# Performance work log

Measured on AMD Instinct MI355X. Metric: run time of the kernel, lower is better.

Reference implementation:

```python
import jax, jax.numpy as jnp
import numpy as np
from jax import lax

N, D, H, C = 4096, 1024, 512, 21  # rois, head feat dim, gcn hidden, n_classes


def setup_inputs() -> dict:
    key = jax.random.key(0)
    ks = jax.random.split(key, 9)
    x1 = jax.random.uniform(ks[0], (N,), minval=0.0, maxval=800.0)
    y1 = jax.random.uniform(ks[1], (N,), minval=0.0, maxval=800.0)
    w = jax.random.uniform(ks[2], (N,), minval=16.0, maxval=256.0)
    h = jax.random.uniform(ks[3], (N,), minval=16.0, maxval=256.0)
    rois = jnp.stack([x1, y1, x1 + w, y1 + h], axis=1)  # [N,4] x1,y1,x2,y2
    pooled_feat = jax.random.normal(ks[4], (N, D))
    Wg1 = jax.random.normal(ks[5], (D, H)) * 0.02
    bg1 = jnp.zeros((H,), jnp.float32)
    Wg2 = jax.random.normal(ks[6], (H, H)) * 0.02
    bg2 = jnp.zeros((H,), jnp.float32)
    W_bbox = jax.random.normal(ks[7], (H, 4 * C)) * 0.001
    b_bbox = jnp.zeros((4 * C,), jnp.float32)
    W_cls = jax.random.normal(ks[8], (H, C)) * 0.01
    b_cls = jnp.zeros((C,), jnp.float32)
    return dict(rois=rois, pooled_feat=pooled_feat, Wg1=Wg1, bg1=bg1, Wg2=Wg2,
                bg2=bg2, W_bbox=W_bbox, b_bbox=b_bbox, W_cls=W_cls, b_cls=b_cls)


def _iou_binary_adj(boxes):
    # bbox_overlaps_batch IoU (Pascal +1 convention), then binarize and zero diag
    x1, y1, x2, y2 = boxes[:, 0], boxes[:, 1], boxes[:, 2], boxes[:, 3]
    area = (x2 - x1 + 1.0) * (y2 - y1 + 1.0)
    iw = jnp.maximum(jnp.minimum(x2[:, None], x2[None, :]) - jnp.maximum(x1[:, None], x1[None, :]) + 1.0, 0.0)
    ih = jnp.maximum(jnp.minimum(y2[:, None], y2[None, :]) - jnp.maximum(y1[:, None], y1[None, :]) + 1.0, 0.0)
    inter = iw * ih
    iou = inter / (area[:, None] + area[None, :] - inter)
    adj = (iou > 0.0).astype(boxes.dtype)
    return adj * (1.0 - jnp.eye(boxes.shape[0], dtype=boxes.dtype))


def _connected_components(adj):
    # jit-friendly replacement for DFS subgraph_split: min-label propagation
    # with pointer jumping (converges in O(log diameter) iterations).
    n = adj.shape[0]
    labels0 = jnp.arange(n, dtype=jnp.int32)
    big = jnp.int32(n)

    def step(labels, _):
        nb = jnp.min(jnp.where(adj > 0.0, labels[None, :], big), axis=1)
        labels = jnp.minimum(labels, nb)
        labels = labels[labels]  # pointer jump
        return labels, None

    labels, _ = lax.scan(step, labels0, None, length=32)
    return labels  # component id per roi (min vertex index in component)


def _cosine_adj(x):
    # pairwise cosine similarity, diag zeroed (matches s != t loop)
    xn = x / jnp.maximum(jnp.linalg.norm(x, axis=1, keepdims=True), 1e-6)
    a = xn @ xn.T
    return a * (1.0 - jnp.eye(x.shape[0], dtype=x.dtype))


def reference(rois, pooled_feat, Wg1, bg1, Wg2, bg2, W_bbox, b_bbox, W_cls, b_cls):
    adj_bin = _iou_binary_adj(rois)          # [N,N] 0/1
    labels = _connected_components(adj_bin)  # [N] int32 subgraph ids
    A = _cosine_adj(pooled_feat)             # [N,N]
    h1 = jax.nn.relu(A @ (pooled_feat @ Wg1) + bg1)  # GCN layer 1
    h2 = jax.nn.relu(A @ (h1 @ Wg2) + bg2)           # GCN layer 2
    bbox_pred = h2 @ W_bbox + b_bbox          # [N, 4*C]
    cls_prob = jax.nn.softmax(h2 @ W_cls + b_cls, axis=1)  # [N, C]
    return labels, cls_prob, bbox_pred
```

## Files before the change

kernel.cpp:

```cpp
#include <hip/hip_runtime.h>
#include <hip/hip_bf16.h>
#include <stdint.h>


typedef __attribute__((ext_vector_type(8))) short short8;
typedef __attribute__((ext_vector_type(4))) float floatx4;

#define BK 64
#define LSTR 72

__device__ __forceinline__ unsigned short bfbits(float f) {
  union { float f; unsigned int i; } u; u.f = f;
  unsigned int r = u.i + 0x7fffu + ((u.i >> 16) & 1);
  return (unsigned short)(r >> 16);
}

template <int MODE>
__global__ __launch_bounds__(256) void gemm64(
    const __hip_bfloat16* __restrict__ P, const __hip_bfloat16* __restrict__ Q,
    int KC, int ld, int N, float* __restrict__ part,
    const float* __restrict__ rinorm, const __hip_bfloat16* __restrict__ ST,
    const float* __restrict__ bias, __hip_bfloat16* __restrict__ outb,
    float* __restrict__ outf, float* __restrict__ cls, const float* __restrict__ bias2) {
  __shared__ short As[2][64 * LSTR];
  __shared__ short Bs[2][64 * LSTR];
  const int tid = threadIdx.x;
  const int w = tid >> 6, lane = tid & 63;
  const size_t m0 = (size_t)blockIdx.y * 64, n0 = (size_t)blockIdx.x * 64;
  const int z = blockIdx.z;

  const int srow = tid >> 2, skoff = (tid & 3) * 16;
  const short* gA = (const short*)P + (m0 + srow) * (size_t)ld + (size_t)z * KC + skoff;
  const short* gB = (const short*)Q + (n0 + srow) * (size_t)ld + (size_t)z * KC + skoff;
  const int soff = srow * LSTR + skoff;

  const int wm = (w >> 1) * 32, wn = (w & 1) * 32;
  const int lr = lane & 15, ko = (lane >> 4) * 8;

  floatx4 acc[2][2];
#pragma unroll
  for (int i = 0; i < 2; ++i)
#pragma unroll
    for (int j = 0; j < 2; ++j) acc[i][j] = (floatx4){0.f, 0.f, 0.f, 0.f};

  const int nIter = KC / BK;
  short8 ra0 = *(const short8*)gA;
  short8 ra1 = *(const short8*)(gA + 8);
  short8 rb0 = *(const short8*)gB;
  short8 rb1 = *(const short8*)(gB + 8);
  *(short8*)&As[0][soff] = ra0;
  *(short8*)&As[0][soff + 8] = ra1;
  *(short8*)&Bs[0][soff] = rb0;
  *(short8*)&Bs[0][soff + 8] = rb1;
  if (nIter > 1) {
    ra0 = *(const short8*)(gA + BK);
    ra1 = *(const short8*)(gA + BK + 8);
    rb0 = *(const short8*)(gB + BK);
    rb1 = *(const short8*)(gB + BK + 8);
  }
  __syncthreads();

  for (int it = 0; it < nIter; ++it) {
    const int cur = it & 1;
    short8 av[2][2], bv[2][2];
#pragma unroll
    for (int ks = 0; ks < 2; ++ks)
#pragma unroll
      for (int t = 0; t < 2; ++t) {
        av[ks][t] = *(const short8*)&As[cur][(wm + t * 16 + lr) * LSTR + ks * 32 + ko];
        bv[ks][t] = *(const short8*)&Bs[cur][(wn + t * 16 + lr) * LSTR + ks * 32 + ko];
      }
    if (it + 1 < nIter) {
      *(short8*)&As[cur ^ 1][soff] = ra0;
      *(short8*)&As[cur ^ 1][soff + 8] = ra1;
      *(short8*)&Bs[cur ^ 1][soff] = rb0;
      *(short8*)&Bs[cur ^ 1][soff + 8] = rb1;
      if (it + 2 < nIter) {
        const int off = (it + 2) * BK;
        ra0 = *(const short8*)(gA + off);
        ra1 = *(const short8*)(gA + off + 8);
        rb0 = *(const short8*)(gB + off);
        rb1 = *(const short8*)(gB + off + 8);
      }
    }
#pragma unroll
    for (int ks = 0; ks < 2; ++ks)
#pragma unroll
      for (int i = 0; i < 2; ++i)
#pragma unroll
        for (int j = 0; j < 2; ++j)
          acc[i][j] = __builtin_amdgcn_mfma_f32_16x16x32_bf16(av[ks][i], bv[ks][j], acc[i][j], 0, 0, 0);
    __syncthreads();
  }

  const size_t MN = (size_t)(gridDim.y * 64) * (size_t)N;
  float* cp = part + (size_t)z * MN;
  float* lg = (float*)&As[0][0];
  const int rb4 = (lane >> 4) * 4;
#pragma unroll
  for (int i = 0; i < 2; ++i)
#pragma unroll
    for (int j = 0; j < 2; ++j)
#pragma unroll
      for (int r = 0; r < 4; ++r) {
        int row = (int)m0 + wm + i * 16 + rb4 + r;
        int col = (int)n0 + wn + j * 16 + lr;
        float v = acc[i][j][r];
        if (MODE == 0) {
          cp[(size_t)row * N + col] = v;
        } else if (MODE == 1) {
          outb[(size_t)row * 4096 + col] = __float2bfloat16(v);
        } else if (MODE == 2) {
          v = rinorm[row] * v - __bfloat162float(ST[(size_t)col * 4096 + row]) + bias[col];
          outb[(size_t)row * 512 + col] = __float2bfloat16(fmaxf(v, 0.f));
        } else {
          if (blockIdx.x == 0) {
            outf[(size_t)row * 84 + col] = v + bias[col];
          } else {
            int lrow = wm + i * 16 + rb4 + r;
            if (col < 84) outf[(size_t)row * 84 + col] = v + bias[col];
            else if (col < 105) lg[lrow * 22 + (col - 84)] = v + bias2[col - 84];
          }
        }
      }
  if (MODE == 3) {
    __syncthreads();
    if (blockIdx.x == 1 && tid < 64) {
      const float* Lr = &lg[tid * 22];
      float m = Lr[0];
#pragma unroll
      for (int k = 1; k < 21; ++k) m = fmaxf(m, Lr[k]);
      float s = 0.f;
      float e[21];
#pragma unroll
      for (int k = 0; k < 21; ++k) { e[k] = expf(Lr[k] - m); s += e[k]; }
      float inv = 1.f / s;
      float* dst = &cls[(m0 + tid) * 21];
#pragma unroll
      for (int k = 0; k < 21; ++k) dst[k] = e[k] * inv;
    }
  }
}

__global__ void k_red0(const float* __restrict__ part, __hip_bfloat16* __restrict__ out,
                       int n, int ns) {
  int i = (blockIdx.x * 256 + threadIdx.x) * 4;
  if (i >= n) return;
  float4 v = *(const float4*)(part + i);
  for (int s = 1; s < ns; ++s) {
    float4 q = *(const float4*)(part + (size_t)s * n + i);
    v.x += q.x; v.y += q.y; v.z += q.z; v.w += q.w;
  }
  out[i] = __float2bfloat16(v.x);
  out[i + 1] = __float2bfloat16(v.y);
  out[i + 2] = __float2bfloat16(v.z);
  out[i + 3] = __float2bfloat16(v.w);
}

__global__ void k_nf_adj(const float* __restrict__ X, __hip_bfloat16* __restrict__ Xb,
                         float* __restrict__ rinorm, const float4* __restrict__ rois,
                         unsigned long long* __restrict__ adj, int* __restrict__ labels) {
  int blk = blockIdx.x, tid = threadIdx.x;
  int lane = tid & 63;
  if (blk < 1024) {
    int wave = (blk * 256 + tid) >> 6;
    const float4* row = (const float4*)(X + (size_t)wave * 1024);
    uint2* orow = (uint2*)((short*)Xb + (size_t)wave * 1024);
    float s = 0.f;
#pragma unroll
    for (int it = 0; it < 4; ++it) {
      float4 p = row[lane + it * 64];
      s += p.x * p.x + p.y * p.y + p.z * p.z + p.w * p.w;
      uint2 q;
      q.x = (unsigned int)bfbits(p.x) | ((unsigned int)bfbits(p.y) << 16);
      q.y = (unsigned int)bfbits(p.z) | ((unsigned int)bfbits(p.w) << 16);
      orow[lane + it * 64] = q;
    }
    for (int o = 32; o; o >>= 1) s += __shfl_down(s, o);
    if (lane == 0) rinorm[wave] = 1.f / fmaxf(sqrtf(s), 1e-6f);
  } else {
    int node = ((blk - 1024) * 256 + tid) >> 6;
    float4 bi = rois[node];
    unsigned long long myword = 0;
    int mn = node;
    for (int w = 0; w < 64; ++w) {
      int j = w * 64 + lane;
      float4 bj = rois[j];
      float iw = fminf(bi.z, bj.z) - fmaxf(bi.x, bj.x) + 1.0f;
      float ih = fminf(bi.w, bj.w) - fmaxf(bi.y, bj.y) + 1.0f;
      bool ov = (iw > 0.f) && (ih > 0.f) && (j != node);
      unsigned long long msk = __ballot(ov);
      if (lane == w) myword = msk;
      if (msk) mn = min(mn, w * 64 + (int)__builtin_ctzll(msk));
    }
    adj[(size_t)node * 64 + lane] = myword;
    if (lane == 0) labels[node] = mn;
  }
}

__global__ void k_prep(const __hip_bfloat16* __restrict__ Xb, const float* __restrict__ rinorm,
                       const float* __restrict__ Wg1, const float* __restrict__ Wg2,
                       const float* __restrict__ Wb, const float* __restrict__ Wc,
                       __hip_bfloat16* __restrict__ XRT, __hip_bfloat16* __restrict__ Wg1T,
                       __hip_bfloat16* __restrict__ Wg2T, __hip_bfloat16* __restrict__ WcatT) {
  __shared__ float s[32][33];
  const int tid = threadIdx.x;
  const int tx = tid & 31, ty = tid >> 5;
  int blk = blockIdx.x;
  if (blk < 4096) {
    int c0 = (blk & 31) * 32, r0 = (blk >> 5) * 32;
#pragma unroll
    for (int k = 0; k < 4; ++k) {
      int r = r0 + ty + k * 8;
      s[ty + k * 8][tx] = __bfloat162float(Xb[(size_t)r * 1024 + c0 + tx]) * rinorm[r];
    }
    __syncthreads();
#pragma unroll
    for (int k = 0; k < 4; ++k)
      XRT[(size_t)(c0 + ty + k * 8) * 4096 + r0 + tx] = __float2bfloat16(s[tx][ty + k * 8]);
  } else if (blk < 4608) {
    int l = blk - 4096;
    int c0 = (l & 15) * 32, r0 = (l >> 4) * 32;
#pragma unroll
    for (int k = 0; k < 4; ++k)
      s[ty + k * 8][tx] = Wg1[(size_t)(r0 + ty + k * 8) * 512 + c0 + tx];
    __syncthreads();
#pragma unroll
    for (int k = 0; k < 4; ++k)
      Wg1T[(size_t)(c0 + ty + k * 8) * 1024 + r0 + tx] = __float2bfloat16(s[tx][ty + k * 8]);
  } else if (blk < 4864) {
    int l = blk - 4608;
    int c0 = (l & 15) * 32, r0 = (l >> 4) * 32;
#pragma unroll
    for (int k = 0; k < 4; ++k)
      s[ty + k * 8][tx] = Wg2[(size_t)(r0 + ty + k * 8) * 512 + c0 + tx];
    __syncthreads();
#pragma unroll
    for (int k = 0; k < 4; ++k)
      Wg2T[(size_t)(c0 + ty + k * 8) * 512 + r0 + tx] = __float2bfloat16(s[tx][ty + k * 8]);
  } else {
    int idx = (blk - 4864) * 256 + tid;
    int r = idx >> 9, k = idx & 511;
    float v = 0.f;
    if (r < 84) v = Wb[(size_t)k * 84 + r];
    else if (r < 105) v = Wc[(size_t)k * 21 + (r - 84)];
    WcatT[idx] = __float2bfloat16(v);
  }
}

__global__ void k_minprop(const unsigned long long* __restrict__ adj, int* __restrict__ labels) {
  int wave = (blockIdx.x * 256 + threadIdx.x) >> 6;
  int lane = threadIdx.x & 63;
  unsigned long long w = adj[(size_t)wave * 64 + lane];
  int m = 0x7fffffff;
  while (w) {
    int b = __builtin_ctzll(w);
    w &= w - 1;
    m = min(m, labels[lane * 64 + b]);
  }
  for (int o = 32; o; o >>= 1) m = min(m, __shfl_down(m, o));
  if (lane == 0 && m < labels[wave]) atomicMin(&labels[wave], m);
}

__global__ void k_jump(int* __restrict__ labels, float* __restrict__ outL) {
  __shared__ int a[4096];
  __shared__ int b[4096];
  int t = threadIdx.x;
  for (int i = t; i < 4096; i += 1024) a[i] = labels[i];
  __syncthreads();
  int* src = a;
  int* dst = b;
  for (int it = 0; it < 12; ++it) {
    for (int i = t; i < 4096; i += 1024) dst[i] = src[src[i]];
    __syncthreads();
    int* tp = src; src = dst; dst = tp;
  }
  for (int i = t; i < 4096; i += 1024) outL[i] = (float)src[i];
}

extern "C" void kernel_launch(void* const* d_in, const int* in_sizes, int n_in,
                              void* d_out, int out_size, void* d_ws, size_t ws_size,
                              hipStream_t stream) {
  const float* rois = (const float*)d_in[0];
  const float* X    = (const float*)d_in[1];
  const float* Wg1  = (const float*)d_in[2];
  const float* bg1  = (const float*)d_in[3];
  const float* Wg2  = (const float*)d_in[4];
  const float* bg2  = (const float*)d_in[5];
  const float* Wb   = (const float*)d_in[6];
  const float* bb   = (const float*)d_in[7];
  const float* Wc   = (const float*)d_in[8];
  const float* bc   = (const float*)d_in[9];

  float* out        = (float*)d_out;
  float* out_labels = out;
  float* out_cls    = out + 4096;
  float* out_bbox   = out + 4096 + 4096 * 21;

  char* p = (char*)d_ws;
  auto carve = [&](size_t bytes) { char* r = p; p += (bytes + 255) & ~(size_t)255; return r; };
  int* labels           = (int*)carve(4096ull * 4);
  float* rinorm         = (float*)carve(4096ull * 4);
  __hip_bfloat16* WcatT = (__hip_bfloat16*)carve(128ull * 512 * 2);
  __hip_bfloat16* Wg2T  = (__hip_bfloat16*)carve(512ull * 512 * 2);
  __hip_bfloat16* Wg1T  = (__hip_bfloat16*)carve(512ull * 1024 * 2);
  __hip_bfloat16* T2T   = (__hip_bfloat16*)carve(512ull * 1024 * 2);
  __hip_bfloat16* h     = (__hip_bfloat16*)carve(4096ull * 512 * 2);
  __hip_bfloat16* ST    = (__hip_bfloat16*)carve(512ull * 4096 * 2);
  __hip_bfloat16* Xb    = (__hip_bfloat16*)carve(4096ull * 1024 * 2);
  __hip_bfloat16* XRT   = (__hip_bfloat16*)carve(1024ull * 4096 * 2);
  unsigned long long* adj = (unsigned long long*)carve(4096ull * 64 * 8);
  float* part           = (float*)carve(16ull * 1024 * 1024);

  k_nf_adj<<<2048, 256, 0, stream>>>(X, Xb, rinorm, (const float4*)rois, adj, labels);
  k_prep<<<5120, 256, 0, stream>>>(Xb, rinorm, Wg1, Wg2, Wb, Wc, XRT, Wg1T, Wg2T, WcatT);
  for (int r = 0; r < 2; ++r) k_minprop<<<1024, 256, 0, stream>>>(adj, labels);
  k_jump<<<1, 1024, 0, stream>>>(labels, out_labels);

  gemm64<1><<<dim3(64, 8), 256, 0, stream>>>(Wg1T, Xb, 1024, 1024, 4096, part,
                                             nullptr, nullptr, nullptr, ST,
                                             nullptr, nullptr, nullptr);
  gemm64<0><<<dim3(16, 8, 4), 256, 0, stream>>>(ST, XRT, 1024, 4096, 1024, part,
                                                nullptr, nullptr, nullptr, nullptr,
                                                nullptr, nullptr, nullptr);
  k_red0<<<512, 256, 0, stream>>>(part, T2T, 512 * 1024, 4);
  gemm64<2><<<dim3(8, 64), 256, 0, stream>>>(Xb, T2T, 1024, 1024, 512, part,
                                             rinorm, ST, bg1, h,
                                             nullptr, nullptr, nullptr);
  gemm64<1><<<dim3(64, 8), 256, 0, stream>>>(Wg2T, h, 512, 512, 4096, part,
                                             nullptr, nullptr, nullptr, ST,
                                             nullptr, nullptr, nullptr);
  gemm64<0><<<dim3(16, 8, 4), 256, 0, stream>>>(ST, XRT, 1024, 4096, 1024, part,
                                                nullptr, nullptr, nullptr, nullptr,
                                                nullptr, nullptr, nullptr);
  k_red0<<<512, 256, 0, stream>>>(part, T2T, 512 * 1024, 4);
  gemm64<2><<<dim3(8, 64), 256, 0, stream>>>(Xb, T2T, 1024, 1024, 512, part,
                                             rinorm, ST, bg2, h,
                                             nullptr, nullptr, nullptr);
  gemm64<3><<<dim3(2, 64), 256, 0, stream>>>(h, WcatT, 512, 512, 128, part,
                                             nullptr, nullptr, bb, nullptr,
                                             out_bbox, out_cls, bc);
}
```

Measured before the change: 204.1 us.

## Stage GEMM tiles with direct global-to-LDS loads and XOR swizzle

```diff
diff --git a/kernel.cpp b/kernel.cpp
--- a/kernel.cpp
+++ b/kernel.cpp
@@ -7,12 +7,17 @@
 typedef __attribute__((ext_vector_type(4))) float floatx4;
 
 #define BK 64
-#define LSTR 72
 
 __device__ __forceinline__ unsigned short bfbits(float f) {
   union { float f; unsigned int i; } u; u.f = f;
   unsigned int r = u.i + 0x7fffu + ((u.i >> 16) & 1);
   return (unsigned short)(r >> 16);
+}
+
+__device__ __forceinline__ void gload16(const short* g, short* l) {
+  __builtin_amdgcn_global_load_lds(
+      (const __attribute__((address_space(1))) void*)(const void*)g,
+      (__attribute__((address_space(3))) void*)(void*)l, 16, 0, 0);
 }
 
 template <int MODE>
@@ -22,20 +27,39 @@
     const float* __restrict__ rinorm, const __hip_bfloat16* __restrict__ ST,
     const float* __restrict__ bias, __hip_bfloat16* __restrict__ outb,
     float* __restrict__ outf, float* __restrict__ cls, const float* __restrict__ bias2) {
-  __shared__ short As[2][64 * LSTR];
-  __shared__ short Bs[2][64 * LSTR];
+  __shared__ __attribute__((aligned(16))) short As[2][64 * 64];
+  __shared__ __attribute__((aligned(16))) short Bs[2][64 * 64];
   const int tid = threadIdx.x;
   const int w = tid >> 6, lane = tid & 63;
   const size_t m0 = (size_t)blockIdx.y * 64, n0 = (size_t)blockIdx.x * 64;
   const int z = blockIdx.z;
 
-  const int srow = tid >> 2, skoff = (tid & 3) * 16;
-  const short* gA = (const short*)P + (m0 + srow) * (size_t)ld + (size_t)z * KC + skoff;
-  const short* gB = (const short*)Q + (n0 + srow) * (size_t)ld + (size_t)z * KC + skoff;
-  const int soff = srow * LSTR + skoff;
+  const int srow = lane >> 3;
+  const int schunk = (lane & 7) ^ srow;
+  const short* gA = (const short*)P + (m0 + w * 16 + srow) * (size_t)ld + (size_t)z * KC + schunk * 8;
+  const short* gB = (const short*)Q + (n0 + w * 16 + srow) * (size_t)ld + (size_t)z * KC + schunk * 8;
+  const short* gA1 = gA + 8 * (size_t)ld;
+  const short* gB1 = gB + 8 * (size_t)ld;
+
+  auto STAGE = [&](int buf, int kk) {
+    gload16(gA + kk, &As[buf][(w * 16) * 64]);
+    gload16(gA1 + kk, &As[buf][(w * 16 + 8) * 64]);
+    gload16(gB + kk, &Bs[buf][(w * 16) * 64]);
+    gload16(gB1 + kk, &Bs[buf][(w * 16 + 8) * 64]);
+  };
 
   const int wm = (w >> 1) * 32, wn = (w & 1) * 32;
-  const int lr = lane & 15, ko = (lane >> 4) * 8;
+  const int lr = lane & 15, g = lane >> 4;
+
+  int offA[2][2], offB[2][2];
+#pragma unroll
+  for (int ks = 0; ks < 2; ++ks)
+#pragma unroll
+    for (int t = 0; t < 2; ++t) {
+      const int pc = ((ks * 4 + g) ^ (lr & 7)) * 8;
+      offA[ks][t] = (wm + t * 16 + lr) * 64 + pc;
+      offB[ks][t] = (wn + t * 16 + lr) * 64 + pc;
+    }
 
   floatx4 acc[2][2];
 #pragma unroll
@@ -44,21 +68,10 @@
     for (int j = 0; j < 2; ++j) acc[i][j] = (floatx4){0.f, 0.f, 0.f, 0.f};
 
   const int nIter = KC / BK;
-  short8 ra0 = *(const short8*)gA;
-  short8 ra1 = *(const short8*)(gA + 8);
-  short8 rb0 = *(const short8*)gB;
-  short8 rb1 = *(const short8*)(gB + 8);
-  *(short8*)&As[0][soff] = ra0;
-  *(short8*)&As[0][soff + 8] = ra1;
-  *(short8*)&Bs[0][soff] = rb0;
-  *(short8*)&Bs[0][soff + 8] = rb1;
-  if (nIter > 1) {
-    ra0 = *(const short8*)(gA + BK);
-    ra1 = *(const short8*)(gA + BK + 8);
-    rb0 = *(const short8*)(gB + BK);
-    rb1 = *(const short8*)(gB + BK + 8);
-  }
-  __syncthreads();
+  STAGE(0, 0);
+  STAGE(1, BK);
+  asm volatile("s_waitcnt vmcnt(4)" ::: "memory");
+  __builtin_amdgcn_s_barrier();
 
   for (int it = 0; it < nIter; ++it) {
     const int cur = it & 1;
@@ -67,22 +80,13 @@
     for (int ks = 0; ks < 2; ++ks)
 #pragma unroll
       for (int t = 0; t < 2; ++t) {
-        av[ks][t] = *(const short8*)&As[cur][(wm + t * 16 + lr) * LSTR + ks * 32 + ko];
-        bv[ks][t] = *(const short8*)&Bs[cur][(wn + t * 16 + lr) * LSTR + ks * 32 + ko];
+        av[ks][t] = *(const short8*)&As[cur][offA[ks][t]];
+        bv[ks][t] = *(const short8*)&Bs[cur][offB[ks][t]];
       }
-    if (it + 1 < nIter) {
-      *(short8*)&As[cur ^ 1][soff] = ra0;
-      *(short8*)&As[cur ^ 1][soff + 8] = ra1;
-      *(short8*)&Bs[cur ^ 1][soff] = rb0;
-      *(short8*)&Bs[cur ^ 1][soff + 8] = rb1;
-      if (it + 2 < nIter) {
-        const int off = (it + 2) * BK;
-        ra0 = *(const short8*)(gA + off);
-        ra1 = *(const short8*)(gA + off + 8);
-        rb0 = *(const short8*)(gB + off);
-        rb1 = *(const short8*)(gB + off + 8);
-      }
-    }
+    asm volatile("s_waitcnt lgkmcnt(0)" ::: "memory");
+    __builtin_amdgcn_sched_barrier(0);
+    __builtin_amdgcn_s_barrier();
+    if (it + 2 < nIter) STAGE(cur, (it + 2) * BK);
 #pragma unroll
     for (int ks = 0; ks < 2; ++ks)
 #pragma unroll
@@ -90,7 +94,11 @@
 #pragma unroll
         for (int j = 0; j < 2; ++j)
           acc[i][j] = __builtin_amdgcn_mfma_f32_16x16x32_bf16(av[ks][i], bv[ks][j], acc[i][j], 0, 0, 0);
-    __syncthreads();
+    if (it + 1 < nIter) {
+      if (it + 2 < nIter) asm volatile("s_waitcnt vmcnt(4)" ::: "memory");
+      else               asm volatile("s_waitcnt vmcnt(0)" ::: "memory");
+      __builtin_amdgcn_s_barrier();
+    }
   }
 
   const size_t MN = (size_t)(gridDim.y * 64) * (size_t)N;
```

Measured after the change: 209.1 us. 1.02x slower.

## Fold connected-component passes into GEMM launches and double GEMM block threads

Applied to the files above, without the earlier changes.

```diff
diff --git a/kernel.cpp b/kernel.cpp
--- a/kernel.cpp
+++ b/kernel.cpp
@@ -15,81 +15,114 @@
   return (unsigned short)(r >> 16);
 }
 
-template <int MODE>
-__global__ __launch_bounds__(256) void gemm64(
+__device__ __forceinline__ void minprop_node(const unsigned long long* adj, int* labels,
+                                             int node, int lane) {
+  unsigned long long w = adj[(size_t)node * 64 + lane];
+  int m = 0x7fffffff;
+  while (w) {
+    int b = __builtin_ctzll(w);
+    w &= w - 1;
+    m = min(m, labels[lane * 64 + b]);
+  }
+  for (int o = 32; o; o >>= 1) m = min(m, __shfl_down(m, o));
+  if (lane == 0 && m < labels[node]) atomicMin(&labels[node], m);
+}
+
+template <int MODE, int CC = 0>
+__global__ __launch_bounds__(512) void gemm64(
     const __hip_bfloat16* __restrict__ P, const __hip_bfloat16* __restrict__ Q,
     int KC, int ld, int N, float* __restrict__ part,
     const float* __restrict__ rinorm, const __hip_bfloat16* __restrict__ ST,
     const float* __restrict__ bias, __hip_bfloat16* __restrict__ outb,
-    float* __restrict__ outf, float* __restrict__ cls, const float* __restrict__ bias2) {
+    float* __restrict__ outf, float* __restrict__ cls, const float* __restrict__ bias2,
+    const unsigned long long* __restrict__ adj, int* __restrict__ labels,
+    float* __restrict__ outL) {
   __shared__ short As[2][64 * LSTR];
   __shared__ short Bs[2][64 * LSTR];
   const int tid = threadIdx.x;
   const int w = tid >> 6, lane = tid & 63;
+
+  if (CC == 1 && blockIdx.y == 8) {
+    int wv = blockIdx.x * 8 + w;
+#pragma unroll
+    for (int k = 0; k < 8; ++k) minprop_node(adj, labels, wv * 8 + k, lane);
+    return;
+  }
+  if (CC == 2 && blockIdx.z == 4) {
+    if (blockIdx.x | blockIdx.y) return;
+    int* a = (int*)&As[0][0];
+    int* b = (int*)&Bs[0][0];
+    for (int i = tid; i < 4096; i += 512) a[i] = labels[i];
+    __syncthreads();
+    int* src = a;
+    int* dst = b;
+    for (int it = 0; it < 12; ++it) {
+      for (int i = tid; i < 4096; i += 512) dst[i] = src[src[i]];
+      __syncthreads();
+      int* tp = src; src = dst; dst = tp;
+    }
+    for (int i = tid; i < 4096; i += 512) outL[i] = (float)src[i];
+    return;
+  }
+
   const size_t m0 = (size_t)blockIdx.y * 64, n0 = (size_t)blockIdx.x * 64;
   const int z = blockIdx.z;
 
-  const int srow = tid >> 2, skoff = (tid & 3) * 16;
-  const short* gA = (const short*)P + (m0 + srow) * (size_t)ld + (size_t)z * KC + skoff;
-  const short* gB = (const short*)Q + (n0 + srow) * (size_t)ld + (size_t)z * KC + skoff;
+  const int sB = tid >> 8;
+  const int t8 = tid & 255;
+  const int srow = t8 >> 2, skoff = (t8 & 3) * 16;
+  const short* gP = (sB ? (const short*)Q + (n0 + srow) * (size_t)ld
+                        : (const short*)P + (m0 + srow) * (size_t)ld)
+                    + (size_t)z * KC + skoff;
+  short* const wb0 = sB ? &Bs[0][0] : &As[0][0];
+  short* const wb1 = sB ? &Bs[1][0] : &As[1][0];
   const int soff = srow * LSTR + skoff;
 
-  const int wm = (w >> 1) * 32, wn = (w & 1) * 32;
+  const int wm = (w >> 1) * 16, wn = (w & 1) * 32;
   const int lr = lane & 15, ko = (lane >> 4) * 8;
 
-  floatx4 acc[2][2];
-#pragma unroll
-  for (int i = 0; i < 2; ++i)
-#pragma unroll
-    for (int j = 0; j < 2; ++j) acc[i][j] = (floatx4){0.f, 0.f, 0.f, 0.f};
+  floatx4 acc[2];
+  acc[0] = (floatx4){0.f, 0.f, 0.f, 0.f};
+  acc[1] = (floatx4){0.f, 0.f, 0.f, 0.f};
 
   const int nIter = KC / BK;
-  short8 ra0 = *(const short8*)gA;
-  short8 ra1 = *(const short8*)(gA + 8);
-  short8 rb0 = *(const short8*)gB;
-  short8 rb1 = *(const short8*)(gB + 8);
-  *(short8*)&As[0][soff] = ra0;
-  *(short8*)&As[0][soff + 8] = ra1;
-  *(short8*)&Bs[0][soff] = rb0;
-  *(short8*)&Bs[0][soff + 8] = rb1;
+  short8 r0 = *(const short8*)gP;
+  short8 r1 = *(const short8*)(gP + 8);
+  *(short8*)&wb0[soff] = r0;
+  *(short8*)&wb0[soff + 8] = r1;
   if (nIter > 1) {
-    ra0 = *(const short8*)(gA + BK);
-    ra1 = *(const short8*)(gA + BK + 8);
-    rb0 = *(const short8*)(gB + BK);
-    rb1 = *(const short8*)(gB + BK + 8);
+    r0 = *(const short8*)(gP + BK);
+    r1 = *(const short8*)(gP + BK + 8);
   }
   __syncthreads();
 
   for (int it = 0; it < nIter; ++it) {
     const int cur = it & 1;
-    short8 av[2][2], bv[2][2];
-#pragma unroll
-    for (int ks = 0; ks < 2; ++ks)
-#pragma unroll
-      for (int t = 0; t < 2; ++t) {
-        av[ks][t] = *(const short8*)&As[cur][(wm + t * 16 + lr) * LSTR + ks * 32 + ko];
-        bv[ks][t] = *(const short8*)&Bs[cur][(wn + t * 16 + lr) * LSTR + ks * 32 + ko];
-      }
+    const short* Ac = &As[cur][0];
+    const short* Bc = &Bs[cur][0];
+    short8 av[2], bv[2][2];
+#pragma unroll
+    for (int ks = 0; ks < 2; ++ks) {
+      av[ks] = *(const short8*)&Ac[(wm + lr) * LSTR + ks * 32 + ko];
+#pragma unroll
+      for (int t = 0; t < 2; ++t)
+        bv[ks][t] = *(const short8*)&Bc[(wn + t * 16 + lr) * LSTR + ks * 32 + ko];
+    }
     if (it + 1 < nIter) {
-      *(short8*)&As[cur ^ 1][soff] = ra0;
-      *(short8*)&As[cur ^ 1][soff + 8] = ra1;
-      *(short8*)&Bs[cur ^ 1][soff] = rb0;
-      *(short8*)&Bs[cur ^ 1][soff + 8] = rb1;
+      short* d = cur ? wb0 : wb1;
+      *(short8*)&d[soff] = r0;
+      *(short8*)&d[soff + 8] = r1;
       if (it + 2 < nIter) {
         const int off = (it + 2) * BK;
-        ra0 = *(const short8*)(gA + off);
-        ra1 = *(const short8*)(gA + off + 8);
-        rb0 = *(const short8*)(gB + off);
-        rb1 = *(const short8*)(gB + off + 8);
+        r0 = *(const short8*)(gP + off);
+        r1 = *(const short8*)(gP + off + 8);
       }
     }
 #pragma unroll
     for (int ks = 0; ks < 2; ++ks)
 #pragma unroll
-      for (int i = 0; i < 2; ++i)
-#pragma unroll
-        for (int j = 0; j < 2; ++j)
-          acc[i][j] = __builtin_amdgcn_mfma_f32_16x16x32_bf16(av[ks][i], bv[ks][j], acc[i][j], 0, 0, 0);
+      for (int j = 0; j < 2; ++j)
+        acc[j] = __builtin_amdgcn_mfma_f32_16x16x32_bf16(av[ks], bv[ks][j], acc[j], 0, 0, 0);
     __syncthreads();
   }
 
@@ -98,31 +131,29 @@
   float* lg = (float*)&As[0][0];
   const int rb4 = (lane >> 4) * 4;
 #pragma unroll
-  for (int i = 0; i < 2; ++i)
-#pragma unroll
-    for (int j = 0; j < 2; ++j)
-#pragma unroll
-      for (int r = 0; r < 4; ++r) {
-        int row = (int)m0 + wm + i * 16 + rb4 + r;
-        int col = (int)n0 + wn + j * 16 + lr;
-        float v = acc[i][j][r];
-        if (MODE == 0) {
-          cp[(size_t)row * N + col] = v;
-        } else if (MODE == 1) {
-          outb[(size_t)row * 4096 + col] = __float2bfloat16(v);
-        } else if (MODE == 2) {
-          v = rinorm[row] * v - __bfloat162float(ST[(size_t)col * 4096 + row]) + bias[col];
-          outb[(size_t)row * 512 + col] = __float2bfloat16(fmaxf(v, 0.f));
+  for (int j = 0; j < 2; ++j)
+#pragma unroll
+    for (int r = 0; r < 4; ++r) {
+      int row = (int)m0 + wm + rb4 + r;
+      int col = (int)n0 + wn + j * 16 + lr;
+      float v = acc[j][r];
+      if (MODE == 0) {
+        cp[(size_t)row * N + col] = v;
+      } else if (MODE == 1) {
+        outb[(size_t)row * 4096 + col] = __float2bfloat16(v);
+      } else if (MODE == 2) {
+        v = rinorm[row] * v - __bfloat162float(ST[(size_t)col * 4096 + row]) + bias[col];
+        outb[(size_t)row * 512 + col] = __float2bfloat16(fmaxf(v, 0.f));
+      } else {
+        if (blockIdx.x == 0) {
+          outf[(size_t)row * 84 + col] = v + bias[col];
         } else {
-          if (blockIdx.x == 0) {
-            outf[(size_t)row * 84 + col] = v + bias[col];
-          } else {
-            int lrow = wm + i * 16 + rb4 + r;
-            if (col < 84) outf[(size_t)row * 84 + col] = v + bias[col];
-            else if (col < 105) lg[lrow * 22 + (col - 84)] = v + bias2[col - 84];
-          }
+          int lrow = wm + rb4 + r;
+          if (col < 84) outf[(size_t)row * 84 + col] = v + bias[col];
+          else if (col < 105) lg[lrow * 22 + (col - 84)] = v + bias2[col - 84];
         }
       }
+    }
   if (MODE == 3) {
     __syncthreads();
     if (blockIdx.x == 1 && tid < 64) {
@@ -202,7 +233,8 @@
                        const float* __restrict__ Wg1, const float* __restrict__ Wg2,
                        const float* __restrict__ Wb, const float* __restrict__ Wc,
                        __hip_bfloat16* __restrict__ XRT, __hip_bfloat16* __restrict__ Wg1T,
-                       __hip_bfloat16* __restrict__ Wg2T, __hip_bfloat16* __restrict__ WcatT) {
+                       __hip_bfloat16* __restrict__ Wg2T, __hip_bfloat16* __restrict__ WcatT,
+                       const unsigned long long* __restrict__ adj, int* __restrict__ labels) {
   __shared__ float s[32][33];
   const int tid = threadIdx.x;
   const int tx = tid & 31, ty = tid >> 5;
@@ -238,44 +270,17 @@
 #pragma unroll
     for (int k = 0; k < 4; ++k)
       Wg2T[(size_t)(c0 + ty + k * 8) * 512 + r0 + tx] = __float2bfloat16(s[tx][ty + k * 8]);
-  } else {
+  } else if (blk < 5120) {
     int idx = (blk - 4864) * 256 + tid;
     int r = idx >> 9, k = idx & 511;
     float v = 0.f;
     if (r < 84) v = Wb[(size_t)k * 84 + r];
     else if (r < 105) v = Wc[(size_t)k * 21 + (r - 84)];
     WcatT[idx] = __float2bfloat16(v);
-  }
-}
-
-__global__ void k_minprop(const unsigned long long* __restrict__ adj, int* __restrict__ labels) {
-  int wave = (blockIdx.x * 256 + threadIdx.x) >> 6;
-  int lane = threadIdx.x & 63;
-  unsigned long long w = adj[(size_t)wave * 64 + lane];
-  int m = 0x7fffffff;
-  while (w) {
-    int b = __builtin_ctzll(w);
-    w &= w - 1;
-    m = min(m, labels[lane * 64 + b]);
-  }
-  for (int o = 32; o; o >>= 1) m = min(m, __shfl_down(m, o));
-  if (lane == 0 && m < labels[wave]) atomicMin(&labels[wave], m);
-}
-
-__global__ void k_jump(int* __restrict__ labels, float* __restrict__ outL) {
-  __shared__ int a[4096];
-  __shared__ int b[4096];
-  int t = threadIdx.x;
-  for (int i = t; i < 4096; i += 1024) a[i] = labels[i];
-  __syncthreads();
-  int* src = a;
-  int* dst = b;
-  for (int it = 0; it < 12; ++it) {
-    for (int i = t; i < 4096; i += 1024) dst[i] = src[src[i]];
-    __syncthreads();
-    int* tp = src; src = dst; dst = tp;
-  }
-  for (int i = t; i < 4096; i += 1024) outL[i] = (float)src[i];
+  } else {
+    int node = (blk - 5120) * 4 + (tid >> 6);
+    minprop_node(adj, labels, node, tid & 63);
+  }
 }
 
 extern "C" void kernel_launch(void* const* d_in, const int* in_sizes, int n_in,
@@ -313,31 +318,37 @@
   float* part           = (float*)carve(16ull * 1024 * 1024);
 
   k_nf_adj<<<2048, 256, 0, stream>>>(X, Xb, rinorm, (const float4*)rois, adj, labels);
-  k_prep<<<5120, 256, 0, stream>>>(Xb, rinorm, Wg1, Wg2, Wb, Wc, XRT, Wg1T, Wg2T, WcatT);
-  for (int r = 0; r < 2; ++r) k_minprop<<<1024, 256, 0, stream>>>(adj, labels);
-  k_jump<<<1, 1024, 0, stream>>>(labels, out_labels);
-
-  gemm64<1><<<dim3(64, 8), 256, 0, stream>>>(Wg1T, Xb, 1024, 1024, 4096, part,
+  k_prep<<<6144, 256, 0, stream>>>(Xb, rinorm, Wg1, Wg2, Wb, Wc, XRT, Wg1T, Wg2T, WcatT,
+                                   adj, labels);
+
+  gemm64<1, 1><<<dim3(64, 9), 512, 0, stream>>>(Wg1T, Xb, 1024, 1024, 4096, part,
+                                                nullptr, nullptr, nullptr, ST,
+                                                nullptr, nullptr, nullptr,
+                                                adj, labels, nullptr);
+  gemm64<0, 2><<<dim3(16, 8, 5), 512, 0, stream>>>(ST, XRT, 1024, 4096, 1024, part,
+                                                   nullptr, nullptr, nullptr, nullptr,
+                                                   nullptr, nullptr, nullptr,
+                                                   nullptr, labels, out_labels);
+  k_red0<<<512, 256, 0, stream>>>(part, T2T, 512 * 1024, 4);
+  gemm64<2><<<dim3(8, 64), 512, 0, stream>>>(Xb, T2T, 1024, 1024, 512, part,
+                                             rinorm, ST, bg1, h,
+                                             nullptr, nullptr, nullptr,
+                                             nullptr, nullptr, nullptr);
+  gemm64<1><<<dim3(64, 8), 512, 0, stream>>>(Wg2T, h, 512, 512, 4096, part,
                                              nullptr, nullptr, nullptr, ST,
+                                             nullptr, nullptr, nullptr,
                                              nullptr, nullptr, nullptr);
-  gemm64<0><<<dim3(16, 8, 4), 256, 0, stream>>>(ST, XRT, 1024, 4096, 1024, part,
+  gemm64<0><<<dim3(16, 8, 4), 512, 0, stream>>>(ST, XRT, 1024, 4096, 1024, part,
                                                 nullptr, nullptr, nullptr, nullptr,
+                                                nullptr, nullptr, nullptr,
                                                 nullptr, nullptr, nullptr);
   k_red0<<<512, 256, 0, stream>>>(part, T2T, 512 * 1024, 4);
-  gemm64<2><<<dim3(8, 64), 256, 0, stream>>>(Xb, T2T, 1024, 1024, 512, part,
-                                             rinorm, ST, bg1, h,
+  gemm64<2><<<dim3(8, 64), 512, 0, stream>>>(Xb, T2T, 1024, 1024, 512, part,
+                                             rinorm, ST, bg2, h,
+                                             nullptr, nullptr, nullptr,
                                              nullptr, nullptr, nullptr);
-  gemm64<1><<<dim3(64, 8), 256, 0, stream>>>(Wg2T, h, 512, 512, 4096, part,
-                                             nullptr, nullptr, nullptr, ST,
+  gemm64<3><<<dim3(2, 64), 512, 0, stream>>>(h, WcatT, 512, 512, 128, part,
+                                             nullptr, nullptr, bb, nullptr,
+                                             out_bbox, out_cls, bc,
                                              nullptr, nullptr, nullptr);
-  gemm64<0><<<dim3(16, 8, 4), 256, 0, stream>>>(ST, XRT, 1024, 4096, 1024, part,
-                                                nullptr, nullptr, nullptr, nullptr,
-                                                nullptr, nullptr, nullptr);
-  k_red0<<<512, 256, 0, stream>>>(part, T2T, 512 * 1024, 4);
-  gemm64<2><<<dim3(8, 64), 256, 0, stream>>>(Xb, T2T, 1024, 1024, 512, part,
-                                             rinorm, ST, bg2, h,
-                                             nullptr, nullptr, nullptr);
-  gemm64<3><<<dim3(2, 64), 256, 0, stream>>>(h, WcatT, 512, 512, 128, part,
-                                             nullptr, nullptr, bb, nullptr,
-                                             out_bbox, out_cls, bc);
-}
+}
```

Result: slower. 225.4 us (+10.5%).

## Fold label propagation and pointer jumping into prep and first GEMM launches

Applied to the files above, without the earlier changes.

```diff
diff --git a/kernel.cpp b/kernel.cpp
--- a/kernel.cpp
+++ b/kernel.cpp
@@ -15,16 +15,42 @@
   return (unsigned short)(r >> 16);
 }
 
-template <int MODE>
+__device__ __forceinline__ void minprop_node(const unsigned long long* adj, int* labels,
+                                             int node, int lane) {
+  unsigned long long w = adj[(size_t)node * 64 + lane];
+  int m = 0x7fffffff;
+  while (w) {
+    int b = __builtin_ctzll(w);
+    w &= w - 1;
+    m = min(m, labels[lane * 64 + b]);
+  }
+  for (int o = 32; o; o >>= 1) m = min(m, __shfl_down(m, o));
+  if (lane == 0 && m < labels[node]) atomicMin(&labels[node], m);
+}
+
+template <int MODE, int CC = 0>
 __global__ __launch_bounds__(256) void gemm64(
     const __hip_bfloat16* __restrict__ P, const __hip_bfloat16* __restrict__ Q,
     int KC, int ld, int N, float* __restrict__ part,
     const float* __restrict__ rinorm, const __hip_bfloat16* __restrict__ ST,
     const float* __restrict__ bias, __hip_bfloat16* __restrict__ outb,
-    float* __restrict__ outf, float* __restrict__ cls, const float* __restrict__ bias2) {
+    float* __restrict__ outf, float* __restrict__ cls, const float* __restrict__ bias2,
+    const int* __restrict__ labelsIn, float* __restrict__ outL) {
   __shared__ short As[2][64 * LSTR];
   __shared__ short Bs[2][64 * LSTR];
   const int tid = threadIdx.x;
+
+  if (CC == 1 && blockIdx.y == 8) {
+    int i = blockIdx.x * 256 + tid;
+    if (i < 4096) {
+      int l = labelsIn[i];
+      int p = labelsIn[l];
+      while (p != l) { l = p; p = labelsIn[l]; }
+      outL[i] = (float)l;
+    }
+    return;
+  }
+
   const int w = tid >> 6, lane = tid & 63;
   const size_t m0 = (size_t)blockIdx.y * 64, n0 = (size_t)blockIdx.x * 64;
   const int z = blockIdx.z;
@@ -93,7 +119,7 @@
     __syncthreads();
   }
 
-  const size_t MN = (size_t)(gridDim.y * 64) * (size_t)N;
+  const size_t MN = (size_t)8 * 64 * (size_t)N;
   float* cp = part + (size_t)z * MN;
   float* lg = (float*)&As[0][0];
   const int rb4 = (lane >> 4) * 4;
@@ -202,7 +228,8 @@
                        const float* __restrict__ Wg1, const float* __restrict__ Wg2,
                        const float* __restrict__ Wb, const float* __restrict__ Wc,
                        __hip_bfloat16* __restrict__ XRT, __hip_bfloat16* __restrict__ Wg1T,
-                       __hip_bfloat16* __restrict__ Wg2T, __hip_bfloat16* __restrict__ WcatT) {
+                       __hip_bfloat16* __restrict__ Wg2T, __hip_bfloat16* __restrict__ WcatT,
+                       const unsigned long long* __restrict__ adj, int* __restrict__ labels) {
   __shared__ float s[32][33];
   const int tid = threadIdx.x;
   const int tx = tid & 31, ty = tid >> 5;
@@ -238,44 +265,22 @@
 #pragma unroll
     for (int k = 0; k < 4; ++k)
       Wg2T[(size_t)(c0 + ty + k * 8) * 512 + r0 + tx] = __float2bfloat16(s[tx][ty + k * 8]);
-  } else {
+  } else if (blk < 5120) {
     int idx = (blk - 4864) * 256 + tid;
     int r = idx >> 9, k = idx & 511;
     float v = 0.f;
     if (r < 84) v = Wb[(size_t)k * 84 + r];
     else if (r < 105) v = Wc[(size_t)k * 21 + (r - 84)];
     WcatT[idx] = __float2bfloat16(v);
+  } else {
+    int node = (blk - 5120) * 4 + (tid >> 6);
+    minprop_node(adj, labels, node, tid & 63);
   }
 }
 
 __global__ void k_minprop(const unsigned long long* __restrict__ adj, int* __restrict__ labels) {
   int wave = (blockIdx.x * 256 + threadIdx.x) >> 6;
-  int lane = threadIdx.x & 63;
-  unsigned long long w = adj[(size_t)wave * 64 + lane];
-  int m = 0x7fffffff;
-  while (w) {
-    int b = __builtin_ctzll(w);
-    w &= w - 1;
-    m = min(m, labels[lane * 64 + b]);
-  }
-  for (int o = 32; o; o >>= 1) m = min(m, __shfl_down(m, o));
-  if (lane == 0 && m < labels[wave]) atomicMin(&labels[wave], m);
-}
-
-__global__ void k_jump(int* __restrict__ labels, float* __restrict__ outL) {
-  __shared__ int a[4096];
-  __shared__ int b[4096];
-  int t = threadIdx.x;
-  for (int i = t; i < 4096; i += 1024) a[i] = labels[i];
-  __syncthreads();
-  int* src = a;
-  int* dst = b;
-  for (int it = 0; it < 12; ++it) {
-    for (int i = t; i < 4096; i += 1024) dst[i] = src[src[i]];
-    __syncthreads();
-    int* tp = src; src = dst; dst = tp;
-  }
-  for (int i = t; i < 4096; i += 1024) outL[i] = (float)src[i];
+  minprop_node(adj, labels, wave, threadIdx.x & 63);
 }
 
 extern "C" void kernel_launch(void* const* d_in, const int* in_sizes, int n_in,
@@ -313,31 +318,38 @@
   float* part           = (float*)carve(16ull * 1024 * 1024);
 
   k_nf_adj<<<2048, 256, 0, stream>>>(X, Xb, rinorm, (const float4*)rois, adj, labels);
-  k_prep<<<5120, 256, 0, stream>>>(Xb, rinorm, Wg1, Wg2, Wb, Wc, XRT, Wg1T, Wg2T, WcatT);
-  for (int r = 0; r < 2; ++r) k_minprop<<<1024, 256, 0, stream>>>(adj, labels);
-  k_jump<<<1, 1024, 0, stream>>>(labels, out_labels);
-
-  gemm64<1><<<dim3(64, 8), 256, 0, stream>>>(Wg1T, Xb, 1024, 1024, 4096, part,
-                                             nullptr, nullptr, nullptr, ST,
-                                             nullptr, nullptr, nullptr);
+  k_prep<<<6144, 256, 0, stream>>>(Xb, rinorm, Wg1, Wg2, Wb, Wc, XRT, Wg1T, Wg2T, WcatT,
+                                   adj, labels);
+  k_minprop<<<1024, 256, 0, stream>>>(adj, labels);
+
+  gemm64<1, 1><<<dim3(64, 9), 256, 0, stream>>>(Wg1T, Xb, 1024, 1024, 4096, part,
+                                                nullptr, nullptr, nullptr, ST,
+                                                nullptr, nullptr, nullptr,
+                                                labels, out_labels);
   gemm64<0><<<dim3(16, 8, 4), 256, 0, stream>>>(ST, XRT, 1024, 4096, 1024, part,
                                                 nullptr, nullptr, nullptr, nullptr,
-                                                nullptr, nullptr, nullptr);
+                                                nullptr, nullptr, nullptr,
+                                                nullptr, nullptr);
   k_red0<<<512, 256, 0, stream>>>(part, T2T, 512 * 1024, 4);
   gemm64<2><<<dim3(8, 64), 256, 0, stream>>>(Xb, T2T, 1024, 1024, 512, part,
                                              rinorm, ST, bg1, h,
-                                             nullptr, nullptr, nullptr);
+                                             nullptr, nullptr, nullptr,
+                                             nullptr, nullptr);
   gemm64<1><<<dim3(64, 8), 256, 0, stream>>>(Wg2T, h, 512, 512, 4096, part,
                                              nullptr, nullptr, nullptr, ST,
-                                             nullptr, nullptr, nullptr);
+                                             nullptr, nullptr, nullptr,
+                                             nullptr, nullptr);
   gemm64<0><<<dim3(16, 8, 4), 256, 0, stream>>>(ST, XRT, 1024, 4096, 1024, part,
                                                 nullptr, nullptr, nullptr, nullptr,
-                                                nullptr, nullptr, nullptr);
+                                                nullptr, nullptr, nullptr,
+                                                nullptr, nullptr);
   k_red0<<<512, 256, 0, stream>>>(part, T2T, 512 * 1024, 4);
   gemm64<2><<<dim3(8, 64), 256, 0, stream>>>(Xb, T2T, 1024, 1024, 512, part,
                                              rinorm, ST, bg2, h,
-                                             nullptr, nullptr, nullptr);
+                                             nullptr, nullptr, nullptr,
+                                             nullptr, nullptr);
   gemm64<3><<<dim3(2, 64), 256, 0, stream>>>(h, WcatT, 512, 512, 128, part,
                                              nullptr, nullptr, bb, nullptr,
-                                             out_bbox, out_cls, bc);
-}
+                                             out_bbox, out_cls, bc,
+                                             nullptr, nullptr);
+}
```

Result: faster. 199.6 us (median of 2 runs) (-2.2%).
